# Kernel tuning notes

Hardware: AMD Instinct MI355X
Metric: run time of the kernel (lower is better)

## Reference

```python
import jax, jax.numpy as jnp
import numpy as np

BANDWIDTH = 1.0
EPS = 1e-20


def setup_inputs() -> dict:
    key = jax.random.key(0)
    k1, k2, k3 = jax.random.split(key, 3)
    test_X = jax.random.normal(k1, (8192, 64), dtype=jnp.float32)
    train_X = jax.random.normal(k2, (16384, 64), dtype=jnp.float32)
    sample_weight = jax.random.uniform(k3, (16384,), dtype=jnp.float32)
    return {"test_X": test_X, "train_X": train_X, "sample_weight": sample_weight}


def reference(test_X, train_X, sample_weight):
    # test_X: [m, d], train_X: [n, d], sample_weight: [n]
    d = train_X.shape[1]
    h = jnp.float32(BANDWIDTH)
    # weights are normalized; with weights, n is treated as 1 => log(n) = 0
    w = sample_weight / jnp.sum(sample_weight)
    Z = 0.5 * d * jnp.log(2.0 * jnp.float32(np.pi)) + d * jnp.log(h)
    # squared L2 distances via expansion (avoids [m, n, d] intermediate)
    t2 = jnp.sum(test_X * test_X, axis=-1)  # [m]
    r2 = jnp.sum(train_X * train_X, axis=-1)  # [n]
    cross = test_X @ train_X.T  # [m, n]
    sq = (t2[:, None] + r2[None, :] - 2.0 * cross) / (h * h)  # [m, n]
    val = -0.5 * sq - Z  # [m, n]
    # weighted, numerically-stable log-sum-exp over train dim
    m_max = jnp.max(val, axis=-1, keepdims=True)  # [m, 1]
    s = jnp.sum(jnp.exp(val - m_max) * w[None, :], axis=-1)  # [m]
    return m_max[:, 0] + jnp.log(s + EPS)
```

## Files before the change

### kernel.cpp

```cpp
#include <hip/hip_runtime.h>
#include <hip/hip_bf16.h>
#include <math.h>

#define M 8192
#define N 16384
#define D 64
#define ZC 58.81206612509905f
#define B0 24.0f
#define LOG2E 1.4426950408889634f
#define HL2E 0.7213475204444817f
#define LN2 0.6931471805599453f

#define PCH 32
#define NCHK (N / PCH)

typedef short v8bf __attribute__((ext_vector_type(8)));
typedef float v16f __attribute__((ext_vector_type(16)));

#define B_AU2  0
#define B_LW2  32768
#define B_PART 98304
#define B_TB   1146880
#define B_TR   2195456

__global__ __launch_bounds__(256) void gk_prep(const float* __restrict__ testX,
                                               const float* __restrict__ trainX,
                                               const float* __restrict__ sw,
                                               __hip_bfloat16* __restrict__ tb,
                                               __hip_bfloat16* __restrict__ rb,
                                               float* __restrict__ au2,
                                               float* __restrict__ lw2) {
    const int tid = threadIdx.x;
    const int e = tid & 7;
    if (blockIdx.x < M / 32) {
        const int row = blockIdx.x * 32 + (tid >> 3);
        const float4* p = reinterpret_cast<const float4*>(testX + (size_t)row * D + e * 8);
        float4 v0 = p[0], v1 = p[1];
        float t2 = v0.x * v0.x + v0.y * v0.y + v0.z * v0.z + v0.w * v0.w
                 + v1.x * v1.x + v1.y * v1.y + v1.z * v1.z + v1.w * v1.w;
        t2 += __shfl_xor(t2, 1, 64);
        t2 += __shfl_xor(t2, 2, 64);
        t2 += __shfl_xor(t2, 4, 64);
        if (e == 0) au2[row] = -HL2E * t2;
        union { __hip_bfloat16 h[8]; uint4 u; } cv;
        cv.h[0] = __float2bfloat16(v0.x * LOG2E);
        cv.h[1] = __float2bfloat16(v0.y * LOG2E);
        cv.h[2] = __float2bfloat16(v0.z * LOG2E);
        cv.h[3] = __float2bfloat16(v0.w * LOG2E);
        cv.h[4] = __float2bfloat16(v1.x * LOG2E);
        cv.h[5] = __float2bfloat16(v1.y * LOG2E);
        cv.h[6] = __float2bfloat16(v1.z * LOG2E);
        cv.h[7] = __float2bfloat16(v1.w * LOG2E);
        *reinterpret_cast<uint4*>(tb + (size_t)row * D + e * 8) = cv.u;
    } else {
        const int row = (blockIdx.x - M / 32) * 32 + (tid >> 3);
        const float4* p = reinterpret_cast<const float4*>(trainX + (size_t)row * D + e * 8);
        float4 v0 = p[0], v1 = p[1];
        float r2 = v0.x * v0.x + v0.y * v0.y + v0.z * v0.z + v0.w * v0.w
                 + v1.x * v1.x + v1.y * v1.y + v1.z * v1.z + v1.w * v1.w;
        r2 += __shfl_xor(r2, 1, 64);
        r2 += __shfl_xor(r2, 2, 64);
        r2 += __shfl_xor(r2, 4, 64);
        if (e == 0) lw2[row] = __builtin_amdgcn_logf(sw[row]) - HL2E * r2 + B0;
        union { __hip_bfloat16 h[8]; uint4 u; } cv;
        cv.h[0] = __float2bfloat16(v0.x);
        cv.h[1] = __float2bfloat16(v0.y);
        cv.h[2] = __float2bfloat16(v0.z);
        cv.h[3] = __float2bfloat16(v0.w);
        cv.h[4] = __float2bfloat16(v1.x);
        cv.h[5] = __float2bfloat16(v1.y);
        cv.h[6] = __float2bfloat16(v1.z);
        cv.h[7] = __float2bfloat16(v1.w);
        *reinterpret_cast<uint4*>(rb + (size_t)row * D + e * 8) = cv.u;
    }
}

__global__ __launch_bounds__(256, 4) void gk_main(const __hip_bfloat16* __restrict__ ta,
                                                  const __hip_bfloat16* __restrict__ tr,
                                                  const float* __restrict__ lw2,
                                                  float* __restrict__ part) {
    __shared__ float red[128 * 65];
    const int tid = threadIdx.x;
    const int w = tid >> 6;
    const int lane = tid & 63;
    const int c = lane & 31;
    const int h = lane >> 5;
    const int mhalf = w & 1;
    const int chalf = w >> 1;

    const int bid = blockIdx.x;
    const int xcd = bid & 7;
    const int j = bid >> 3;
    const int chunk = xcd * 4 + (j & 3);
    const int m0 = (j >> 2) * 128;
    const int n0 = chunk * NCHK;

    v8bf af[2][4];
    const __hip_bfloat16* ar = ta + (size_t)(m0 + mhalf * 64 + c) * D;
#pragma unroll
    for (int t = 0; t < 4; ++t) {
        af[0][t] = *reinterpret_cast<const v8bf*>(ar + (2 * t + h) * 8);
        af[1][t] = *reinterpret_cast<const v8bf*>(ar + 32 * D + (2 * t + h) * 8);
    }

    float srun[2][16];
#pragma unroll
    for (int ms = 0; ms < 2; ++ms)
#pragma unroll
        for (int r = 0; r < 16; ++r) srun[ms][r] = 0.f;

    for (int jt = 0; jt < 8; ++jt) {
        const int nt = n0 + chalf * 256 + jt * 32;
        const float lwv = lw2[nt + c];
        const __hip_bfloat16* br = tr + (size_t)(nt + c) * D;
        v8bf bf[4];
#pragma unroll
        for (int t = 0; t < 4; ++t)
            bf[t] = *reinterpret_cast<const v8bf*>(br + (2 * t + h) * 8);
#pragma unroll
        for (int ms = 0; ms < 2; ++ms) {
            v16f acc;
#pragma unroll
            for (int r = 0; r < 16; ++r) acc[r] = lwv;
#pragma unroll
            for (int t = 0; t < 4; ++t)
                acc = __builtin_amdgcn_mfma_f32_32x32x16_bf16(af[ms][t], bf[t], acc, 0, 0, 0);
#pragma unroll
            for (int r = 0; r < 16; ++r)
                srun[ms][r] += __builtin_amdgcn_exp2f(acc[r]);
        }
    }

#pragma unroll
    for (int ms = 0; ms < 2; ++ms)
#pragma unroll
        for (int r = 0; r < 16; ++r) {
            int row = mhalf * 64 + ms * 32 + (r & 3) + 8 * (r >> 2) + 4 * h;
            red[row * 65 + chalf * 32 + c] = srun[ms][r];
        }
    __syncthreads();
    if (tid < 128) {
        float G = 0.f;
#pragma unroll
        for (int c2 = 0; c2 < 64; ++c2) G += red[tid * 65 + c2];
        part[(size_t)chunk * M + m0 + tid] = G;
    }
}

__global__ __launch_bounds__(256) void gk_merge(const float* __restrict__ part,
                                                const float* __restrict__ au2,
                                                const float* __restrict__ sw,
                                                float* __restrict__ out) {
    __shared__ float red[256];
    const int tid = threadIdx.x;
    float s = 0.f;
    const float4* p4 = reinterpret_cast<const float4*>(sw);
    for (int i = tid; i < N / 4; i += 256) {
        float4 v = p4[i];
        s += v.x + v.y + v.z + v.w;
    }
    red[tid] = s;
    __syncthreads();
    for (int off = 128; off > 0; off >>= 1) {
        if (tid < off) red[tid] += red[tid + off];
        __syncthreads();
    }
    const float W = red[0];

    const int r = blockIdx.x * 256 + tid;
    float G = 0.f;
#pragma unroll
    for (int p = 0; p < PCH; ++p) G += part[(size_t)p * M + r];
    out[r] = LN2 * (au2[r] + __builtin_amdgcn_logf(fmaxf(G, 1e-30f)) - B0
                   - __builtin_amdgcn_logf(W)) - ZC;
}

extern "C" void kernel_launch(void* const* d_in, const int* in_sizes, int n_in,
                              void* d_out, int out_size, void* d_ws, size_t ws_size,
                              hipStream_t stream) {
    const float* testX  = (const float*)d_in[0];
    const float* trainX = (const float*)d_in[1];
    const float* sw     = (const float*)d_in[2];
    float* out = (float*)d_out;
    char* wsb = (char*)d_ws;

    float* au2  = (float*)(wsb + B_AU2);
    float* lw2  = (float*)(wsb + B_LW2);
    float* part = (float*)(wsb + B_PART);
    __hip_bfloat16* tb = (__hip_bfloat16*)(wsb + B_TB);
    __hip_bfloat16* rb = (__hip_bfloat16*)(wsb + B_TR);

    gk_prep<<<M / 32 + N / 32, 256, 0, stream>>>(testX, trainX, sw, tb, rb, au2, lw2);
    gk_main<<<(M / 128) * PCH, 256, 0, stream>>>(tb, rb, lw2, part);
    gk_merge<<<M / 256, 256, 0, stream>>>(part, au2, sw, out);
}
```

Before: 109.6 us.

## Double-buffer train tiles via global_load_lds DMA and enlarge row block

Each wave now owns 64 test rows of a 256-row block and streams the whole 512-row train chunk through a per-wave double-buffered LDS ring filled with direct global-to-LDS loads, so the next tile's load overlaps the current tile's MFMA and exp work. The block-level LDS reduction and barrier are replaced by cross-lane shuffle reductions, with lane 0 of each half writing the partials. The grid halves, and each wave does twice as many tiles, which cuts parallelism and relies on hand-coded waitcnt values being correct.

```diff
diff --git a/kernel.cpp b/kernel.cpp
--- a/kernel.cpp
+++ b/kernel.cpp
@@ -13,6 +13,8 @@
 
 #define PCH 32
 #define NCHK (N / PCH)
+#define RB 256
+#define NTILES (NCHK / 32)
 
 typedef short v8bf __attribute__((ext_vector_type(8)));
 typedef float v16f __attribute__((ext_vector_type(16)));
@@ -75,59 +77,99 @@
     }
 }
 
+__device__ __forceinline__ void dma16(const void* g, void* l) {
+    __builtin_amdgcn_global_load_lds(
+        (const __attribute__((address_space(1))) unsigned int*)g,
+        (__attribute__((address_space(3))) unsigned int*)l, 16, 0, 0);
+}
+
+__device__ __forceinline__ void dma_tile32(const __hip_bfloat16* tr, int nt,
+                                           char* dst, int lane) {
+#pragma unroll
+    for (int i = 0; i < 4; ++i) {
+        const __hip_bfloat16* gp =
+            tr + (size_t)(nt + i * 8 + (lane & 7)) * D + (lane >> 3) * 8;
+        dma16(gp, dst + i * 1024);
+    }
+}
+
+__device__ __forceinline__ void compute_tile32(const char* myb, float lwv,
+                                               const v8bf af[2][4],
+                                               float srun[2][16], int c, int h) {
+    v8bf bf[4];
+#pragma unroll
+    for (int t = 0; t < 4; ++t)
+        bf[t] = *reinterpret_cast<const v8bf*>(
+            myb + (c >> 3) * 1024 + (2 * t + h) * 128 + (c & 7) * 16);
+    v16f a0, a1;
+#pragma unroll
+    for (int r = 0; r < 16; ++r) { a0[r] = lwv; a1[r] = lwv; }
+#pragma unroll
+    for (int t = 0; t < 4; ++t)
+        a0 = __builtin_amdgcn_mfma_f32_32x32x16_bf16(af[0][t], bf[t], a0, 0, 0, 0);
+#pragma unroll
+    for (int t = 0; t < 4; ++t)
+        a1 = __builtin_amdgcn_mfma_f32_32x32x16_bf16(af[1][t], bf[t], a1, 0, 0, 0);
+#pragma unroll
+    for (int r = 0; r < 16; ++r) {
+        srun[0][r] += __builtin_amdgcn_exp2f(a0[r]);
+        srun[1][r] += __builtin_amdgcn_exp2f(a1[r]);
+    }
+}
+
 __global__ __launch_bounds__(256, 4) void gk_main(const __hip_bfloat16* __restrict__ ta,
                                                   const __hip_bfloat16* __restrict__ tr,
                                                   const float* __restrict__ lw2,
                                                   float* __restrict__ part) {
-    __shared__ float red[128 * 65];
+    __shared__ __align__(16) char smem[32768];
     const int tid = threadIdx.x;
     const int w = tid >> 6;
     const int lane = tid & 63;
     const int c = lane & 31;
     const int h = lane >> 5;
-    const int mhalf = w & 1;
-    const int chalf = w >> 1;
 
     const int bid = blockIdx.x;
-    const int xcd = bid & 7;
-    const int j = bid >> 3;
-    const int chunk = xcd * 4 + (j & 3);
-    const int m0 = (j >> 2) * 128;
+    const int chunk = (bid & 7) * 4 + ((bid >> 3) & 3);
+    const int m0 = (bid >> 5) * RB;
     const int n0 = chunk * NCHK;
 
+    char* const myb0 = smem + w * 8192;
+    char* const myb1 = myb0 + 4096;
+
+    const __hip_bfloat16* ar = ta + (size_t)(m0 + w * 64 + c) * D;
     v8bf af[2][4];
-    const __hip_bfloat16* ar = ta + (size_t)(m0 + mhalf * 64 + c) * D;
 #pragma unroll
     for (int t = 0; t < 4; ++t) {
         af[0][t] = *reinterpret_cast<const v8bf*>(ar + (2 * t + h) * 8);
         af[1][t] = *reinterpret_cast<const v8bf*>(ar + 32 * D + (2 * t + h) * 8);
     }
 
+    dma_tile32(tr, n0, myb0, lane);
+    float lw0 = lw2[n0 + c];
+    dma_tile32(tr, n0 + 32, myb1, lane);
+    float lw1 = lw2[n0 + 32 + c];
+
     float srun[2][16];
 #pragma unroll
     for (int ms = 0; ms < 2; ++ms)
 #pragma unroll
         for (int r = 0; r < 16; ++r) srun[ms][r] = 0.f;
 
-    for (int jt = 0; jt < 8; ++jt) {
-        const int nt = n0 + chalf * 256 + jt * 32;
-        const float lwv = lw2[nt + c];
-        const __hip_bfloat16* br = tr + (size_t)(nt + c) * D;
-        v8bf bf[4];
-#pragma unroll
-        for (int t = 0; t < 4; ++t)
-            bf[t] = *reinterpret_cast<const v8bf*>(br + (2 * t + h) * 8);
-#pragma unroll
-        for (int ms = 0; ms < 2; ++ms) {
-            v16f acc;
-#pragma unroll
-            for (int r = 0; r < 16; ++r) acc[r] = lwv;
-#pragma unroll
-            for (int t = 0; t < 4; ++t)
-                acc = __builtin_amdgcn_mfma_f32_32x32x16_bf16(af[ms][t], bf[t], acc, 0, 0, 0);
-#pragma unroll
-            for (int r = 0; r < 16; ++r)
-                srun[ms][r] += __builtin_amdgcn_exp2f(acc[r]);
+#pragma unroll
+    for (int t = 0; t < NTILES; ++t) {
+        if (t < NTILES - 2) __builtin_amdgcn_s_waitcnt(0x0F75);
+        else                __builtin_amdgcn_s_waitcnt(0x0F70);
+
+        const char* myb = (t & 1) ? myb1 : myb0;
+        const float lwv = (t & 1) ? lw1 : lw0;
+        compute_tile32(myb, lwv, af, srun, c, h);
+
+        if (t + 2 < NTILES) {
+            const int nt2 = n0 + (t + 2) * 32;
+            char* dst = (t & 1) ? myb1 : myb0;
+            dma_tile32(tr, nt2, dst, lane);
+            if (t & 1) lw1 = lw2[nt2 + c];
+            else       lw0 = lw2[nt2 + c];
         }
     }
 
@@ -135,15 +177,22 @@
     for (int ms = 0; ms < 2; ++ms)
 #pragma unroll
         for (int r = 0; r < 16; ++r) {
-            int row = mhalf * 64 + ms * 32 + (r & 3) + 8 * (r >> 2) + 4 * h;
-            red[row * 65 + chalf * 32 + c] = srun[ms][r];
+            float v = srun[ms][r];
+            v += __shfl_xor(v, 1, 64);
+            v += __shfl_xor(v, 2, 64);
+            v += __shfl_xor(v, 4, 64);
+            v += __shfl_xor(v, 8, 64);
+            v += __shfl_xor(v, 16, 64);
+            srun[ms][r] = v;
         }
-    __syncthreads();
-    if (tid < 128) {
-        float G = 0.f;
-#pragma unroll
-        for (int c2 = 0; c2 < 64; ++c2) G += red[tid * 65 + c2];
-        part[(size_t)chunk * M + m0 + tid] = G;
+    if (c == 0) {
+#pragma unroll
+        for (int ms = 0; ms < 2; ++ms)
+#pragma unroll
+            for (int r = 0; r < 16; ++r) {
+                const int row = w * 64 + ms * 32 + (r & 3) + 8 * (r >> 2) + 4 * h;
+                part[(size_t)chunk * M + m0 + row] = srun[ms][r];
+            }
     }
 }
 
@@ -191,6 +240,6 @@
     __hip_bfloat16* rb = (__hip_bfloat16*)(wsb + B_TR);
 
     gk_prep<<<M / 32 + N / 32, 256, 0, stream>>>(testX, trainX, sw, tb, rb, au2, lw2);
-    gk_main<<<(M / 128) * PCH, 256, 0, stream>>>(tb, rb, lw2, part);
+    gk_main<<<(M / RB) * PCH, 256, 0, stream>>>(tb, rb, lw2, part);
     gk_merge<<<M / 256, 256, 0, stream>>>(part, au2, sw, out);
 }
```

Result: slower. 165.5 us (+51.0%).
